# Kernel optimization log

Measured on AMD Instinct MI355X. Metric: run time of the kernel, lower is better.

Reference implementation:

```python
import jax, jax.numpy as jnp
import numpy as np

N, C, H, W = 16, 512, 64, 64
C_BAR, C_HAT = 64, 256


def max_pool2(t):
    # t: [n, c, h, w] -> [n, c, h//2, w//2] via 2x2 max pool
    n, c, h, w = t.shape
    return t.reshape(n, c, h // 2, 2, w // 2, 2).max(axis=(3, 5))


def setup_inputs() -> dict:
    key = jax.random.key(0)
    ks = jax.random.split(key, 6)
    x = jax.random.normal(ks[0], (N, C, H, W), dtype=jnp.float32)
    # 1x1 conv weights stored as [out_channels, in_channels]
    w_theta = jax.random.normal(ks[1], (C_BAR, C), dtype=jnp.float32) * 0.02
    w_phi = jax.random.normal(ks[2], (C_BAR, C), dtype=jnp.float32) * 0.02
    w_g = jax.random.normal(ks[3], (C_HAT, C), dtype=jnp.float32) * 0.02
    w_o = jax.random.normal(ks[4], (C, C_HAT), dtype=jnp.float32) * 0.02
    # gamma initialized to zero in the module; use a small nonzero value so the
    # attention path contributes to the output (and to gradients).
    gamma = jnp.full((1,), 0.1, dtype=jnp.float32)
    return {"x": x, "w_theta": w_theta, "w_phi": w_phi, "w_g": w_g,
            "w_o": w_o, "gamma": gamma}


def reference(x, w_theta, w_phi, w_g, w_o, gamma):
    n, c, h, w = x.shape
    hw, hw4 = h * w, (h * w) // 4
    # 1x1 conv projections (pure channel GEMMs)
    g_x = jnp.einsum('nchw,oc->nohw', x, w_g)          # [n, c_hat, h, w]
    g_x = max_pool2(g_x).reshape(n, -1, hw4)            # [n, c_hat, hw/4]
    phi_x = jnp.einsum('nchw,oc->nohw', x, w_phi)       # [n, c_bar, h, w]
    phi_x = max_pool2(phi_x).reshape(n, -1, hw4)        # [n, c_bar, hw/4]
    theta_x = jnp.einsum('nchw,oc->nohw', x, w_theta).reshape(n, -1, hw)  # [n, c_bar, hw]
    # bmm -> softmax -> bmm
    scores = jnp.einsum('nds,ndt->nst', theta_x, phi_x)  # [n, hw, hw/4]
    attn = jax.nn.softmax(scores, axis=-1)
    y = jnp.einsum('ndt,nst->nds', g_x, attn)            # [n, c_hat, hw]
    y = y.reshape(n, -1, h, w)
    o = jnp.einsum('nchw,oc->nohw', y, w_o)              # [n, c, h, w]
    return gamma[0] * o + x
```

## Files before the change

kernel.cpp:

```cpp
#include <hip/hip_runtime.h>
#include <stdint.h>

typedef unsigned short u16;
typedef u16   us8 __attribute__((ext_vector_type(8)));
typedef __bf16 bf8 __attribute__((ext_vector_type(8)));
typedef float f4  __attribute__((ext_vector_type(4)));

__device__ __forceinline__ u16 f2bf(float f) {
    uint32_t u = __builtin_bit_cast(uint32_t, f);
    uint32_t r = (u + 0x7fffu + ((u >> 16) & 1u)) >> 16;
    return (u16)r;
}
__device__ __forceinline__ float bf2f(u16 s) {
    uint32_t u = ((uint32_t)s) << 16;
    return __builtin_bit_cast(float, u);
}
__device__ __forceinline__ f4 mfma16(bf8 a, bf8 b, f4 c) {
    return __builtin_amdgcn_mfma_f32_16x16x32_bf16(a, b, c, 0, 0, 0);
}

__global__ __launch_bounds__(256) void proj_gemm(
    const float* __restrict__ w_theta, const float* __restrict__ w_phi,
    const float* __restrict__ w_g, const float* __restrict__ x,
    u16* __restrict__ P)
{
    const int nt = blockIdx.x;
    const int mt = blockIdx.y;
    const int nb = blockIdx.z;
    const int tid = threadIdx.x;
    const int wave = tid >> 6, lane = tid & 63;
    const int quad = lane >> 4, l15 = lane & 15;
    const int wm = (wave >> 1) * 32, wn = (wave & 1) * 64;
    const int s0 = nt * 128;

    const float* A; int m_off;
    if (mt == 0)      { A = w_theta; m_off = 0; }
    else if (mt == 1) { A = w_phi;   m_off = 0; }
    else              { A = w_g;     m_off = (mt - 2) * 64; }

    const float* Bx = x + (size_t)nb * 512 * 4096;

    __shared__ u16 a_lds[64 * 40];
    __shared__ u16 b_lds[128 * 40];

    f4 acc[2][4];
    f4 z = {0.f, 0.f, 0.f, 0.f};
    for (int i = 0; i < 2; i++) for (int j = 0; j < 4; j++) acc[i][j] = z;

    for (int k0 = 0; k0 < 512; k0 += 32) {
        {
            int m = tid >> 2, kq = (tid & 3) * 8;
            const float* src = A + (size_t)(m_off + m) * 512 + k0 + kq;
            float4 f0 = *(const float4*)(src);
            float4 f1 = *(const float4*)(src + 4);
            us8 v;
            v[0]=f2bf(f0.x); v[1]=f2bf(f0.y); v[2]=f2bf(f0.z); v[3]=f2bf(f0.w);
            v[4]=f2bf(f1.x); v[5]=f2bf(f1.y); v[6]=f2bf(f1.z); v[7]=f2bf(f1.w);
            *(us8*)&a_lds[m * 40 + kq] = v;
        }
        {
            int k = tid >> 3, c0 = (tid & 7) * 16;
            const float* src = Bx + (size_t)(k0 + k) * 4096 + s0 + c0;
            for (int jj = 0; jj < 4; jj++) {
                float4 f = *(const float4*)(src + jj * 4);
                int c = c0 + jj * 4;
                b_lds[(c + 0) * 40 + k] = f2bf(f.x);
                b_lds[(c + 1) * 40 + k] = f2bf(f.y);
                b_lds[(c + 2) * 40 + k] = f2bf(f.z);
                b_lds[(c + 3) * 40 + k] = f2bf(f.w);
            }
        }
        __syncthreads();
        bf8 af[2], bfr[4];
        for (int i = 0; i < 2; i++)
            af[i] = __builtin_bit_cast(bf8, *(const us8*)&a_lds[(wm + i*16 + l15)*40 + quad*8]);
        for (int j = 0; j < 4; j++)
            bfr[j] = __builtin_bit_cast(bf8, *(const us8*)&b_lds[(wn + j*16 + l15)*40 + quad*8]);
        for (int i = 0; i < 2; i++)
            for (int j = 0; j < 4; j++)
                acc[i][j] = mfma16(af[i], bfr[j], acc[i][j]);
        __syncthreads();
    }
    for (int i = 0; i < 2; i++) {
        int row = mt * 64 + wm + i * 16 + quad * 4;
        for (int j = 0; j < 4; j++) {
            int col = s0 + wn + j * 16 + l15;
            for (int rr = 0; rr < 4; rr++)
                P[((size_t)nb * 384 + row + rr) * 4096 + col] = f2bf(acc[i][j][rr]);
        }
    }
}

__global__ __launch_bounds__(256) void theta_trans(
    const u16* __restrict__ P, u16* __restrict__ thetaT)
{
    int n = blockIdx.y, s0 = blockIdx.x * 64;
    int tid = threadIdx.x;
    int s_loc = tid & 63, d0 = (tid >> 6) * 16;
    const u16* base = P + (size_t)n * 384 * 4096 + s0 + s_loc;
    us8 v0, v1;
    for (int i = 0; i < 8; i++) v0[i] = base[(size_t)(d0 + i) * 4096];
    for (int i = 0; i < 8; i++) v1[i] = base[(size_t)(d0 + 8 + i) * 4096];
    u16* dst = thetaT + ((size_t)n * 4096 + s0 + s_loc) * 64 + d0;
    *(us8*)dst = v0;
    *(us8*)(dst + 8) = v1;
}

__global__ __launch_bounds__(256) void phi_pool(
    const u16* __restrict__ P, u16* __restrict__ phiT)
{
    int n = blockIdx.y, t0 = blockIdx.x * 64;
    int tid = threadIdx.x;
    int t_loc = tid & 63, d0 = (tid >> 6) * 16;
    int t = t0 + t_loc;
    int h2 = t >> 5, w2 = t & 31;
    size_t s00 = (size_t)h2 * 128 + w2 * 2;
    const u16* base = P + ((size_t)n * 384 + 64) * 4096 + s00;
    us8 v0, v1;
    for (int i = 0; i < 16; i++) {
        const u16* r = base + (size_t)(d0 + i) * 4096;
        float m = fmaxf(fmaxf(bf2f(r[0]), bf2f(r[1])),
                        fmaxf(bf2f(r[64]), bf2f(r[65])));
        u16 us = f2bf(m);
        if (i < 8) v0[i] = us; else v1[i - 8] = us;
    }
    u16* dst = phiT + ((size_t)n * 1024 + t) * 64 + d0;
    *(us8*)dst = v0;
    *(us8*)(dst + 8) = v1;
}

__global__ __launch_bounds__(256) void g_pool(
    const u16* __restrict__ P, u16* __restrict__ gP)
{
    int n = blockIdx.y, d2 = blockIdx.x;
    int tid = threadIdx.x;
    const u16* base = P + ((size_t)n * 384 + 128 + d2) * 4096;
    u16* dst = gP + ((size_t)n * 256 + d2) * 1024;
    for (int p = 0; p < 4; p++) {
        int t = p * 256 + tid;
        int h2 = t >> 5, w2 = t & 31;
        size_t s00 = (size_t)h2 * 128 + w2 * 2;
        float m = fmaxf(fmaxf(bf2f(base[s00]), bf2f(base[s00 + 1])),
                        fmaxf(bf2f(base[s00 + 64]), bf2f(base[s00 + 65])));
        dst[t] = f2bf(m);
    }
}

__global__ __launch_bounds__(256) void attn_kernel(
    const u16* __restrict__ thetaT, const u16* __restrict__ phiT,
    const u16* __restrict__ gP, u16* __restrict__ yT)
{
    int n = blockIdx.y;
    int tid = threadIdx.x;
    int wave = tid >> 6, lane = tid & 63, quad = lane >> 4, l15 = lane & 15;
    int q0 = blockIdx.x * 64 + wave * 16;

    __shared__ u16 phi_lds[32 * 72];
    __shared__ u16 g_lds[256 * 40];
    __shared__ u16 p_lds[4][16 * 40];

    const u16* th = thetaT + ((size_t)n * 4096 + q0 + l15) * 64 + quad * 8;
    bf8 a0 = __builtin_bit_cast(bf8, *(const us8*)(th));
    bf8 a1 = __builtin_bit_cast(bf8, *(const us8*)(th + 32));

    f4 z = {0.f, 0.f, 0.f, 0.f};
    f4 acc[16];
    for (int b = 0; b < 16; b++) acc[b] = z;
    float lsum[4] = {0.f, 0.f, 0.f, 0.f};

    for (int tc = 0; tc < 1024; tc += 32) {
        {
            int t_loc = tid >> 3, d0 = (tid & 7) * 8;
            *(us8*)&phi_lds[t_loc * 72 + d0] =
                *(const us8*)(phiT + ((size_t)n * 1024 + tc + t_loc) * 64 + d0);
        }
        {
            const u16* src = gP + ((size_t)n * 256 + tid) * 1024 + tc;
            *(us8*)&g_lds[tid * 40 + 0]  = *(const us8*)(src);
            *(us8*)&g_lds[tid * 40 + 8]  = *(const us8*)(src + 8);
            *(us8*)&g_lds[tid * 40 + 16] = *(const us8*)(src + 16);
            *(us8*)&g_lds[tid * 40 + 24] = *(const us8*)(src + 24);
        }
        __syncthreads();

        for (int tt = 0; tt < 32; tt += 16) {
            bf8 b0 = __builtin_bit_cast(bf8, *(const us8*)&phi_lds[(tt + l15) * 72 + quad * 8]);
            bf8 b1 = __builtin_bit_cast(bf8, *(const us8*)&phi_lds[(tt + l15) * 72 + 32 + quad * 8]);
            f4 s = mfma16(a0, b0, z);
            s = mfma16(a1, b1, s);
            for (int rr = 0; rr < 4; rr++) {
                float p = __expf(s[rr]);
                lsum[rr] += p;
                p_lds[wave][(quad * 4 + rr) * 40 + tt + l15] = f2bf(p);
            }
        }
        bf8 ap = __builtin_bit_cast(bf8, *(const us8*)&p_lds[wave][l15 * 40 + quad * 8]);
        for (int b = 0; b < 16; b++) {
            bf8 bg = __builtin_bit_cast(bf8, *(const us8*)&g_lds[(b * 16 + l15) * 40 + quad * 8]);
            acc[b] = mfma16(ap, bg, acc[b]);
        }
        __syncthreads();
    }

    for (int rr = 0; rr < 4; rr++) {
        float v = lsum[rr];
        v += __shfl_xor(v, 1);
        v += __shfl_xor(v, 2);
        v += __shfl_xor(v, 4);
        v += __shfl_xor(v, 8);
        lsum[rr] = 1.0f / v;
    }
    for (int b = 0; b < 16; b++)
        for (int rr = 0; rr < 4; rr++) {
            size_t row = (size_t)n * 4096 + q0 + quad * 4 + rr;
            yT[row * 256 + b * 16 + l15] = f2bf(acc[b][rr] * lsum[rr]);
        }
}

__global__ __launch_bounds__(256) void oproj_gemm(
    const float* __restrict__ w_o, const u16* __restrict__ yT,
    const float* __restrict__ x, const float* __restrict__ gamma,
    float* __restrict__ out)
{
    const int nt = blockIdx.x;
    const int mt = blockIdx.y;
    const int nb = blockIdx.z;
    const int tid = threadIdx.x;
    const int wave = tid >> 6, lane = tid & 63;
    const int quad = lane >> 4, l15 = lane & 15;
    const int wm = (wave >> 1) * 32, wn = (wave & 1) * 64;
    const int s0 = nt * 128;

    __shared__ u16 a_lds[64 * 40];
    __shared__ u16 b_lds[128 * 40];

    f4 acc[2][4];
    f4 z = {0.f, 0.f, 0.f, 0.f};
    for (int i = 0; i < 2; i++) for (int j = 0; j < 4; j++) acc[i][j] = z;

    for (int k0 = 0; k0 < 256; k0 += 32) {
        {
            int m = tid >> 2, kq = (tid & 3) * 8;
            const float* src = w_o + (size_t)(mt * 64 + m) * 256 + k0 + kq;
            float4 f0 = *(const float4*)(src);
            float4 f1 = *(const float4*)(src + 4);
            us8 v;
            v[0]=f2bf(f0.x); v[1]=f2bf(f0.y); v[2]=f2bf(f0.z); v[3]=f2bf(f0.w);
            v[4]=f2bf(f1.x); v[5]=f2bf(f1.y); v[6]=f2bf(f1.z); v[7]=f2bf(f1.w);
            *(us8*)&a_lds[m * 40 + kq] = v;
        }
        {
            int s_loc = tid >> 1, kq = (tid & 1) * 16;
            const u16* src = yT + ((size_t)nb * 4096 + s0 + s_loc) * 256 + k0 + kq;
            *(us8*)&b_lds[s_loc * 40 + kq]     = *(const us8*)(src);
            *(us8*)&b_lds[s_loc * 40 + kq + 8] = *(const us8*)(src + 8);
        }
        __syncthreads();
        bf8 af[2], bfr[4];
        for (int i = 0; i < 2; i++)
            af[i] = __builtin_bit_cast(bf8, *(const us8*)&a_lds[(wm + i*16 + l15)*40 + quad*8]);
        for (int j = 0; j < 4; j++)
            bfr[j] = __builtin_bit_cast(bf8, *(const us8*)&b_lds[(wn + j*16 + l15)*40 + quad*8]);
        for (int i = 0; i < 2; i++)
            for (int j = 0; j < 4; j++)
                acc[i][j] = mfma16(af[i], bfr[j], acc[i][j]);
        __syncthreads();
    }
    float g0 = gamma[0];
    for (int i = 0; i < 2; i++) {
        int c = mt * 64 + wm + i * 16 + quad * 4;
        for (int j = 0; j < 4; j++) {
            int s = s0 + wn + j * 16 + l15;
            for (int rr = 0; rr < 4; rr++) {
                size_t idx = ((size_t)nb * 512 + c + rr) * 4096 + s;
                out[idx] = g0 * acc[i][j][rr] + x[idx];
            }
        }
    }
}

extern "C" void kernel_launch(void* const* d_in, const int* in_sizes, int n_in,
                              void* d_out, int out_size, void* d_ws, size_t ws_size,
                              hipStream_t stream)
{
    (void)in_sizes; (void)n_in; (void)out_size; (void)ws_size;
    const float* x       = (const float*)d_in[0];
    const float* w_theta = (const float*)d_in[1];
    const float* w_phi   = (const float*)d_in[2];
    const float* w_g     = (const float*)d_in[3];
    const float* w_o     = (const float*)d_in[4];
    const float* gamma   = (const float*)d_in[5];
    float* out = (float*)d_out;

    char* ws = (char*)d_ws;
    u16* P      = (u16*)(ws);
    u16* thetaT = (u16*)(ws + 50331648);
    u16* phiT   = (u16*)(ws + 58720256);
    u16* gP     = (u16*)(ws + 60817408);
    u16* yT     = (u16*)(ws + 69205760);

    proj_gemm  <<<dim3(32, 6, 16),  256, 0, stream>>>(w_theta, w_phi, w_g, x, P);
    theta_trans<<<dim3(64, 16),     256, 0, stream>>>(P, thetaT);
    phi_pool   <<<dim3(16, 16),     256, 0, stream>>>(P, phiT);
    g_pool     <<<dim3(256, 16),    256, 0, stream>>>(P, gP);
    attn_kernel<<<dim3(64, 16),     256, 0, stream>>>(thetaT, phiT, gP, yT);
    oproj_gemm <<<dim3(32, 8, 16),  256, 0, stream>>>(w_o, yT, x, gamma, out);
}
```

Measured before the change: 476.9 us.

## Pre-transpose x to bf16, pre-convert weights, emit projections in position-major layout

Adds a kernel that transposes and converts x to bf16 [n, s, c] and another that converts all weights to bf16 once per call. The projection GEMM then loads contiguous bf16 tiles, uses a larger 128x128 tile, and writes a position-major PT buffer. Attention reads theta directly from PT, which removes the theta transpose kernel. The pooling kernels now read vectorized rows, and g pooling gains an LDS transpose. The aim is to cut strided scalar loads and the per-tile fp32-to-bf16 conversion inside the GEMMs, at the cost of an extra full pass over x and scattered 2-byte stores in the PT epilogue.

```diff
diff --git a/kernel.cpp b/kernel.cpp
--- a/kernel.cpp
+++ b/kernel.cpp
@@ -2,6 +2,7 @@
 #include <stdint.h>
 
 typedef unsigned short u16;
+typedef u16   us4 __attribute__((ext_vector_type(4)));
 typedef u16   us8 __attribute__((ext_vector_type(8)));
 typedef __bf16 bf8 __attribute__((ext_vector_type(8)));
 typedef float f4  __attribute__((ext_vector_type(4)));
@@ -18,136 +19,164 @@
 __device__ __forceinline__ f4 mfma16(bf8 a, bf8 b, f4 c) {
     return __builtin_amdgcn_mfma_f32_16x16x32_bf16(a, b, c, 0, 0, 0);
 }
-
-__global__ __launch_bounds__(256) void proj_gemm(
+__device__ __forceinline__ u16 max4bf(u16 a, u16 b, u16 c, u16 d) {
+    float m = fmaxf(fmaxf(bf2f(a), bf2f(b)), fmaxf(bf2f(c), bf2f(d)));
+    return f2bf(m);
+}
+
+__global__ __launch_bounds__(256) void xt_kernel(
+    const float* __restrict__ x, u16* __restrict__ Xt)
+{
+    const int s0 = blockIdx.x * 64, c0 = blockIdx.y * 64, n = blockIdx.z;
+    const int tid = threadIdx.x;
+    __shared__ u16 lds[64 * 72];
+
+    {
+        int c_loc = tid & 63, s_seg = (tid >> 6) * 16;
+        const float* src = x + ((size_t)n * 512 + c0 + c_loc) * 4096 + s0 + s_seg;
+        for (int i4 = 0; i4 < 4; i4++) {
+            float4 f = *(const float4*)(src + i4 * 4);
+            int s = s_seg + i4 * 4;
+            lds[(s + 0) * 72 + c_loc] = f2bf(f.x);
+            lds[(s + 1) * 72 + c_loc] = f2bf(f.y);
+            lds[(s + 2) * 72 + c_loc] = f2bf(f.z);
+            lds[(s + 3) * 72 + c_loc] = f2bf(f.w);
+        }
+    }
+    __syncthreads();
+    {
+        int s_loc = tid >> 2, c_seg = (tid & 3) * 16;
+        u16* dst = Xt + ((size_t)n * 4096 + s0 + s_loc) * 512 + c0 + c_seg;
+        *(us8*)(dst)     = *(const us8*)&lds[s_loc * 72 + c_seg];
+        *(us8*)(dst + 8) = *(const us8*)&lds[s_loc * 72 + c_seg + 8];
+    }
+}
+
+__global__ __launch_bounds__(256) void wconv_kernel(
     const float* __restrict__ w_theta, const float* __restrict__ w_phi,
-    const float* __restrict__ w_g, const float* __restrict__ x,
-    u16* __restrict__ P)
-{
-    const int nt = blockIdx.x;
-    const int mt = blockIdx.y;
+    const float* __restrict__ w_g, const float* __restrict__ w_o,
+    u16* __restrict__ Wall_bf, u16* __restrict__ Wo_bf)
+{
+    int base = (blockIdx.x * 256 + threadIdx.x) * 4;
+    const float* src; u16* dst;
+    if (base < 32768)       { src = w_theta + base;          dst = Wall_bf + base; }
+    else if (base < 65536)  { src = w_phi + (base - 32768);  dst = Wall_bf + base; }
+    else if (base < 196608) { src = w_g + (base - 65536);    dst = Wall_bf + base; }
+    else                    { src = w_o + (base - 196608);   dst = Wo_bf + (base - 196608); }
+    float4 f = *(const float4*)src;
+    us4 v; v[0] = f2bf(f.x); v[1] = f2bf(f.y); v[2] = f2bf(f.z); v[3] = f2bf(f.w);
+    *(us4*)dst = v;
+}
+
+__global__ __launch_bounds__(256) void projT_gemm(
+    const u16* __restrict__ Xt, const u16* __restrict__ Wall_bf,
+    u16* __restrict__ PT)
+{
+    const int s0 = blockIdx.x * 128;
+    const int r0 = blockIdx.y * 128;
     const int nb = blockIdx.z;
     const int tid = threadIdx.x;
     const int wave = tid >> 6, lane = tid & 63;
     const int quad = lane >> 4, l15 = lane & 15;
-    const int wm = (wave >> 1) * 32, wn = (wave & 1) * 64;
-    const int s0 = nt * 128;
-
-    const float* A; int m_off;
-    if (mt == 0)      { A = w_theta; m_off = 0; }
-    else if (mt == 1) { A = w_phi;   m_off = 0; }
-    else              { A = w_g;     m_off = (mt - 2) * 64; }
-
-    const float* Bx = x + (size_t)nb * 512 * 4096;
-
-    __shared__ u16 a_lds[64 * 40];
+    const int wm = (wave >> 1) * 64, wn = (wave & 1) * 64;
+
+    __shared__ u16 a_lds[128 * 40];
     __shared__ u16 b_lds[128 * 40];
 
-    f4 acc[2][4];
+    f4 acc[4][4];
     f4 z = {0.f, 0.f, 0.f, 0.f};
-    for (int i = 0; i < 2; i++) for (int j = 0; j < 4; j++) acc[i][j] = z;
+    for (int i = 0; i < 4; i++) for (int j = 0; j < 4; j++) acc[i][j] = z;
+
+    const u16* Abase = Xt + ((size_t)nb * 4096 + s0) * 512;
+    const int m = tid >> 1, kseg = (tid & 1) * 16;
 
     for (int k0 = 0; k0 < 512; k0 += 32) {
-        {
-            int m = tid >> 2, kq = (tid & 3) * 8;
-            const float* src = A + (size_t)(m_off + m) * 512 + k0 + kq;
-            float4 f0 = *(const float4*)(src);
-            float4 f1 = *(const float4*)(src + 4);
-            us8 v;
-            v[0]=f2bf(f0.x); v[1]=f2bf(f0.y); v[2]=f2bf(f0.z); v[3]=f2bf(f0.w);
-            v[4]=f2bf(f1.x); v[5]=f2bf(f1.y); v[6]=f2bf(f1.z); v[7]=f2bf(f1.w);
-            *(us8*)&a_lds[m * 40 + kq] = v;
-        }
-        {
-            int k = tid >> 3, c0 = (tid & 7) * 16;
-            const float* src = Bx + (size_t)(k0 + k) * 4096 + s0 + c0;
-            for (int jj = 0; jj < 4; jj++) {
-                float4 f = *(const float4*)(src + jj * 4);
-                int c = c0 + jj * 4;
-                b_lds[(c + 0) * 40 + k] = f2bf(f.x);
-                b_lds[(c + 1) * 40 + k] = f2bf(f.y);
-                b_lds[(c + 2) * 40 + k] = f2bf(f.z);
-                b_lds[(c + 3) * 40 + k] = f2bf(f.w);
-            }
-        }
-        __syncthreads();
-        bf8 af[2], bfr[4];
-        for (int i = 0; i < 2; i++)
-            af[i] = __builtin_bit_cast(bf8, *(const us8*)&a_lds[(wm + i*16 + l15)*40 + quad*8]);
+        *(us8*)&a_lds[m * 40 + kseg]     = *(const us8*)(Abase + (size_t)m * 512 + k0 + kseg);
+        *(us8*)&a_lds[m * 40 + kseg + 8] = *(const us8*)(Abase + (size_t)m * 512 + k0 + kseg + 8);
+        *(us8*)&b_lds[m * 40 + kseg]     = *(const us8*)(Wall_bf + (size_t)(r0 + m) * 512 + k0 + kseg);
+        *(us8*)&b_lds[m * 40 + kseg + 8] = *(const us8*)(Wall_bf + (size_t)(r0 + m) * 512 + k0 + kseg + 8);
+        __syncthreads();
+        bf8 af[4], bfr[4];
+        for (int i = 0; i < 4; i++)
+            af[i]  = __builtin_bit_cast(bf8, *(const us8*)&a_lds[(wm + i*16 + l15)*40 + quad*8]);
         for (int j = 0; j < 4; j++)
             bfr[j] = __builtin_bit_cast(bf8, *(const us8*)&b_lds[(wn + j*16 + l15)*40 + quad*8]);
-        for (int i = 0; i < 2; i++)
+        for (int i = 0; i < 4; i++)
             for (int j = 0; j < 4; j++)
                 acc[i][j] = mfma16(af[i], bfr[j], acc[i][j]);
         __syncthreads();
     }
-    for (int i = 0; i < 2; i++) {
-        int row = mt * 64 + wm + i * 16 + quad * 4;
-        for (int j = 0; j < 4; j++) {
-            int col = s0 + wn + j * 16 + l15;
-            for (int rr = 0; rr < 4; rr++)
-                P[((size_t)nb * 384 + row + rr) * 4096 + col] = f2bf(acc[i][j][rr]);
-        }
-    }
-}
-
-__global__ __launch_bounds__(256) void theta_trans(
-    const u16* __restrict__ P, u16* __restrict__ thetaT)
-{
-    int n = blockIdx.y, s0 = blockIdx.x * 64;
-    int tid = threadIdx.x;
-    int s_loc = tid & 63, d0 = (tid >> 6) * 16;
-    const u16* base = P + (size_t)n * 384 * 4096 + s0 + s_loc;
-    us8 v0, v1;
-    for (int i = 0; i < 8; i++) v0[i] = base[(size_t)(d0 + i) * 4096];
-    for (int i = 0; i < 8; i++) v1[i] = base[(size_t)(d0 + 8 + i) * 4096];
-    u16* dst = thetaT + ((size_t)n * 4096 + s0 + s_loc) * 64 + d0;
-    *(us8*)dst = v0;
-    *(us8*)(dst + 8) = v1;
-}
-
-__global__ __launch_bounds__(256) void phi_pool(
-    const u16* __restrict__ P, u16* __restrict__ phiT)
+    for (int i = 0; i < 4; i++) {
+        int s_idx = s0 + wm + i * 16 + quad * 4;
+        for (int rr = 0; rr < 4; rr++) {
+            u16* dst = PT + ((size_t)nb * 4096 + s_idx + rr) * 384 + r0 + wn + l15;
+            for (int j = 0; j < 4; j++)
+                dst[j * 16] = f2bf(acc[i][j][rr]);
+        }
+    }
+}
+
+__global__ __launch_bounds__(256) void phi_pool2(
+    const u16* __restrict__ PT, u16* __restrict__ phiT)
 {
     int n = blockIdx.y, t0 = blockIdx.x * 64;
     int tid = threadIdx.x;
-    int t_loc = tid & 63, d0 = (tid >> 6) * 16;
+    int t_loc = tid >> 2, d0 = (tid & 3) * 16;
     int t = t0 + t_loc;
     int h2 = t >> 5, w2 = t & 31;
-    size_t s00 = (size_t)h2 * 128 + w2 * 2;
-    const u16* base = P + ((size_t)n * 384 + 64) * 4096 + s00;
-    us8 v0, v1;
-    for (int i = 0; i < 16; i++) {
-        const u16* r = base + (size_t)(d0 + i) * 4096;
-        float m = fmaxf(fmaxf(bf2f(r[0]), bf2f(r[1])),
-                        fmaxf(bf2f(r[64]), bf2f(r[65])));
-        u16 us = f2bf(m);
-        if (i < 8) v0[i] = us; else v1[i - 8] = us;
+    int s00 = h2 * 128 + w2 * 2;
+    const u16* base = PT + ((size_t)n * 4096) * 384 + 64 + d0;
+    us8 r[4][2];
+    int soff[4] = {s00, s00 + 1, s00 + 64, s00 + 65};
+    for (int p = 0; p < 4; p++) {
+        r[p][0] = *(const us8*)(base + (size_t)soff[p] * 384);
+        r[p][1] = *(const us8*)(base + (size_t)soff[p] * 384 + 8);
+    }
+    us8 o0, o1;
+    for (int i = 0; i < 8; i++) {
+        o0[i] = max4bf(r[0][0][i], r[1][0][i], r[2][0][i], r[3][0][i]);
+        o1[i] = max4bf(r[0][1][i], r[1][1][i], r[2][1][i], r[3][1][i]);
     }
     u16* dst = phiT + ((size_t)n * 1024 + t) * 64 + d0;
-    *(us8*)dst = v0;
-    *(us8*)(dst + 8) = v1;
-}
-
-__global__ __launch_bounds__(256) void g_pool(
-    const u16* __restrict__ P, u16* __restrict__ gP)
-{
-    int n = blockIdx.y, d2 = blockIdx.x;
+    *(us8*)dst = o0;
+    *(us8*)(dst + 8) = o1;
+}
+
+__global__ __launch_bounds__(256) void g_poolT(
+    const u16* __restrict__ PT, u16* __restrict__ gP)
+{
+    int t0 = blockIdx.x * 64, d0 = blockIdx.y * 64, n = blockIdx.z;
     int tid = threadIdx.x;
-    const u16* base = P + ((size_t)n * 384 + 128 + d2) * 4096;
-    u16* dst = gP + ((size_t)n * 256 + d2) * 1024;
-    for (int p = 0; p < 4; p++) {
-        int t = p * 256 + tid;
+    __shared__ u16 lds[64 * 72];
+
+    {
+        int t_loc = tid & 63, dseg = (tid >> 6) * 16;
+        int t = t0 + t_loc;
         int h2 = t >> 5, w2 = t & 31;
-        size_t s00 = (size_t)h2 * 128 + w2 * 2;
-        float m = fmaxf(fmaxf(bf2f(base[s00]), bf2f(base[s00 + 1])),
-                        fmaxf(bf2f(base[s00 + 64]), bf2f(base[s00 + 65])));
-        dst[t] = f2bf(m);
+        int s00 = h2 * 128 + w2 * 2;
+        const u16* base = PT + ((size_t)n * 4096) * 384 + 128 + d0 + dseg;
+        us8 r[4][2];
+        int soff[4] = {s00, s00 + 1, s00 + 64, s00 + 65};
+        for (int p = 0; p < 4; p++) {
+            r[p][0] = *(const us8*)(base + (size_t)soff[p] * 384);
+            r[p][1] = *(const us8*)(base + (size_t)soff[p] * 384 + 8);
+        }
+        for (int i = 0; i < 8; i++) {
+            lds[(dseg + i) * 72 + t_loc]     = max4bf(r[0][0][i], r[1][0][i], r[2][0][i], r[3][0][i]);
+            lds[(dseg + 8 + i) * 72 + t_loc] = max4bf(r[0][1][i], r[1][1][i], r[2][1][i], r[3][1][i]);
+        }
+    }
+    __syncthreads();
+    {
+        int d_loc = tid >> 2, t_seg = (tid & 3) * 16;
+        u16* dst = gP + ((size_t)n * 256 + d0 + d_loc) * 1024 + t0 + t_seg;
+        *(us8*)(dst)     = *(const us8*)&lds[d_loc * 72 + t_seg];
+        *(us8*)(dst + 8) = *(const us8*)&lds[d_loc * 72 + t_seg + 8];
     }
 }
 
 __global__ __launch_bounds__(256) void attn_kernel(
-    const u16* __restrict__ thetaT, const u16* __restrict__ phiT,
+    const u16* __restrict__ PT, const u16* __restrict__ phiT,
     const u16* __restrict__ gP, u16* __restrict__ yT)
 {
     int n = blockIdx.y;
@@ -159,7 +188,7 @@
     __shared__ u16 g_lds[256 * 40];
     __shared__ u16 p_lds[4][16 * 40];
 
-    const u16* th = thetaT + ((size_t)n * 4096 + q0 + l15) * 64 + quad * 8;
+    const u16* th = PT + ((size_t)n * 4096 + q0 + l15) * 384 + quad * 8;
     bf8 a0 = __builtin_bit_cast(bf8, *(const us8*)(th));
     bf8 a1 = __builtin_bit_cast(bf8, *(const us8*)(th + 32));
 
@@ -218,7 +247,7 @@
 }
 
 __global__ __launch_bounds__(256) void oproj_gemm(
-    const float* __restrict__ w_o, const u16* __restrict__ yT,
+    const u16* __restrict__ Wo_bf, const u16* __restrict__ yT,
     const float* __restrict__ x, const float* __restrict__ gamma,
     float* __restrict__ out)
 {
@@ -241,13 +270,8 @@
     for (int k0 = 0; k0 < 256; k0 += 32) {
         {
             int m = tid >> 2, kq = (tid & 3) * 8;
-            const float* src = w_o + (size_t)(mt * 64 + m) * 256 + k0 + kq;
-            float4 f0 = *(const float4*)(src);
-            float4 f1 = *(const float4*)(src + 4);
-            us8 v;
-            v[0]=f2bf(f0.x); v[1]=f2bf(f0.y); v[2]=f2bf(f0.z); v[3]=f2bf(f0.w);
-            v[4]=f2bf(f1.x); v[5]=f2bf(f1.y); v[6]=f2bf(f1.z); v[7]=f2bf(f1.w);
-            *(us8*)&a_lds[m * 40 + kq] = v;
+            *(us8*)&a_lds[m * 40 + kq] =
+                *(const us8*)(Wo_bf + (size_t)(mt * 64 + m) * 256 + k0 + kq);
         }
         {
             int s_loc = tid >> 1, kq = (tid & 1) * 16;
@@ -293,16 +317,19 @@
     float* out = (float*)d_out;
 
     char* ws = (char*)d_ws;
-    u16* P      = (u16*)(ws);
-    u16* thetaT = (u16*)(ws + 50331648);
-    u16* phiT   = (u16*)(ws + 58720256);
-    u16* gP     = (u16*)(ws + 60817408);
-    u16* yT     = (u16*)(ws + 69205760);
-
-    proj_gemm  <<<dim3(32, 6, 16),  256, 0, stream>>>(w_theta, w_phi, w_g, x, P);
-    theta_trans<<<dim3(64, 16),     256, 0, stream>>>(P, thetaT);
-    phi_pool   <<<dim3(16, 16),     256, 0, stream>>>(P, phiT);
-    g_pool     <<<dim3(256, 16),    256, 0, stream>>>(P, gP);
-    attn_kernel<<<dim3(64, 16),     256, 0, stream>>>(thetaT, phiT, gP, yT);
-    oproj_gemm <<<dim3(32, 8, 16),  256, 0, stream>>>(w_o, yT, x, gamma, out);
-}
+    u16* Xt      = (u16*)(ws);
+    u16* yT      = (u16*)(ws);
+    u16* phiT    = (u16*)(ws + 33554432);
+    u16* gP      = (u16*)(ws + 35651584);
+    u16* Wall_bf = (u16*)(ws + 67108864);
+    u16* Wo_bf   = (u16*)(ws + 67502080);
+    u16* PT      = (u16*)(ws + 67764224);
+
+    xt_kernel  <<<dim3(64, 8, 16), 256, 0, stream>>>(x, Xt);
+    wconv_kernel<<<320, 256, 0, stream>>>(w_theta, w_phi, w_g, w_o, Wall_bf, Wo_bf);
+    projT_gemm <<<dim3(32, 3, 16), 256, 0, stream>>>(Xt, Wall_bf, PT);
+    phi_pool2  <<<dim3(16, 16),    256, 0, stream>>>(PT, phiT);
+    g_poolT    <<<dim3(16, 4, 16), 256, 0, stream>>>(PT, gP);
+    attn_kernel<<<dim3(64, 16),    256, 0, stream>>>(PT, phiT, gP, yT);
+    oproj_gemm <<<dim3(32, 8, 16), 256, 0, stream>>>(Wo_bf, yT, x, gamma, out);
+}
```

After: 453.9 us. 1.05x faster.
